# Performance work log

Measured on AMD Instinct MI355X. Metric: run time of the kernel, lower is better.

Reference implementation:

```python
import jax, jax.numpy as jnp
import numpy as np


def setup_inputs() -> dict:
    key = jax.random.key(0)
    k1, k2, k3, k4, k5 = jax.random.split(key, 5)
    N, IN, OUT = 4096, 2048, 2048
    return {
        "input": jax.random.normal(k1, (N, IN), dtype=jnp.float32),
        "weight_mu": jax.random.normal(k2, (OUT, IN), dtype=jnp.float32) * 0.25,
        "weight_rho": jax.random.normal(k3, (OUT, IN), dtype=jnp.float32) - 5.0,
        "eps_weight": jax.random.normal(k4, (OUT, IN), dtype=jnp.float32),
        "bias": jax.random.normal(k5, (OUT,), dtype=jnp.float32) * 0.02,
    }


def reference(input, weight_mu, weight_rho, eps_weight, bias):
    # Effective weight: mu + softplus(rho) * eps   (log1p(exp(rho)) == softplus)
    w = weight_mu + jax.nn.softplus(weight_rho) * eps_weight  # [out, in]
    # F.linear: input @ w.T + bias
    return jnp.einsum("ni,oi->no", input, w) + bias
```

## Files before the change

### kernel.cpp

```cpp
#include <hip/hip_runtime.h>
#include <stdint.h>

typedef __bf16 bf16x8 __attribute__((ext_vector_type(8)));
typedef float f32x4 __attribute__((ext_vector_type(4)));
typedef float float4v __attribute__((ext_vector_type(4)));
typedef unsigned short u16x8 __attribute__((ext_vector_type(8)));

__device__ __forceinline__ unsigned short f2bf(float f) {
    unsigned u = __float_as_uint(f);
    u += 0x7fffu + ((u >> 16) & 1u);
    return (unsigned short)(u >> 16);
}

__device__ __forceinline__ float softplus(float x) {
    return fmaxf(x, 0.0f) + __logf(1.0f + __expf(-fabsf(x)));
}

__device__ __forceinline__ void gl_lds16(const void* gptr, void* lptr) {
    auto g = reinterpret_cast<const __attribute__((address_space(1))) void*>(
        reinterpret_cast<uintptr_t>(gptr));
    auto l = reinterpret_cast<__attribute__((address_space(3))) void*>(
        reinterpret_cast<uintptr_t>(lptr));
    __builtin_amdgcn_global_load_lds(g, l, 16, 0, 0);
}

__global__ void prep_kernel(const float* __restrict__ in,
                            const float* __restrict__ mu,
                            const float* __restrict__ rho,
                            const float* __restrict__ eps,
                            unsigned short* __restrict__ in_bf,
                            unsigned short* __restrict__ w_bf,
                            int nIn8, int nW8) {
    int i = blockIdx.x * blockDim.x + threadIdx.x;
    if (i < nIn8) {
        const float4v* p = (const float4v*)in + (size_t)i * 2;
        float4v a = p[0], b = p[1];
        u16x8 r;
        r[0] = f2bf(a[0]); r[1] = f2bf(a[1]); r[2] = f2bf(a[2]); r[3] = f2bf(a[3]);
        r[4] = f2bf(b[0]); r[5] = f2bf(b[1]); r[6] = f2bf(b[2]); r[7] = f2bf(b[3]);
        ((u16x8*)in_bf)[i] = r;
    } else {
        int j = i - nIn8;
        if (j >= nW8) return;
        const float4v* pm = (const float4v*)mu  + (size_t)j * 2;
        const float4v* pr = (const float4v*)rho + (size_t)j * 2;
        const float4v* pe = (const float4v*)eps + (size_t)j * 2;
        float4v m0 = pm[0], m1 = pm[1];
        float4v r0 = pr[0], r1 = pr[1];
        float4v e0 = pe[0], e1 = pe[1];
        u16x8 r;
        r[0] = f2bf(m0[0] + softplus(r0[0]) * e0[0]);
        r[1] = f2bf(m0[1] + softplus(r0[1]) * e0[1]);
        r[2] = f2bf(m0[2] + softplus(r0[2]) * e0[2]);
        r[3] = f2bf(m0[3] + softplus(r0[3]) * e0[3]);
        r[4] = f2bf(m1[0] + softplus(r1[0]) * e1[0]);
        r[5] = f2bf(m1[1] + softplus(r1[1]) * e1[1]);
        r[6] = f2bf(m1[2] + softplus(r1[2]) * e1[2]);
        r[7] = f2bf(m1[3] + softplus(r1[3]) * e1[3]);
        ((u16x8*)w_bf)[j] = r;
    }
}

#define BM 256
#define BN 128
#define KC 32
#define BUF_U 12288

__global__ __launch_bounds__(512, 4)
void gemm_bt_kernel(const unsigned short* __restrict__ A,
                    const unsigned short* __restrict__ B,
                    const float* __restrict__ bias,
                    float* __restrict__ C,
                    int M, int N, int K) {
    __shared__ unsigned short lds[2][BUF_U];

    const int t      = threadIdx.x;
    const int lane   = t & 63;
    const int wave   = t >> 6;
    const int lane16 = lane & 15;
    const int quad   = lane >> 4;
    const int wm     = wave & 3;
    const int wn     = wave >> 2;

    const int m0 = blockIdx.y * BM;
    const int n0 = blockIdx.x * BN;

    const int r   = t >> 2;
    const int key = (t >> 3) & 3;
    const int kgs = ((t & 3) ^ key) * 8;

    const unsigned short* aP0 = A + (size_t)(m0 + r)       * K + kgs;
    const unsigned short* aP1 = A + (size_t)(m0 + 128 + r) * K + kgs;
    const unsigned short* bP  = B + (size_t)(n0 + r)       * K + kgs;

    f32x4 acc[4][4] = {};

    auto stage = [&](int buf, int it) {
        const int k0 = it * KC;
        gl_lds16(aP0 + k0, &lds[buf][t * 8]);
        gl_lds16(aP1 + k0, &lds[buf][4096 + t * 8]);
        gl_lds16(bP  + k0, &lds[buf][8192 + t * 8]);
    };

    const int sw = (lane16 >> 1) & 3;
    const int ra = (wm * 64 + lane16) * KC + ((quad ^ sw) * 8);
    const int rb = 8192 + (wn * 64 + lane16) * KC + ((quad ^ sw) * 8);

    const int nit = K / KC;
    stage(0, 0);
    __syncthreads();

    auto body = [&](int cur, int it) {
        const unsigned short* la = lds[cur];
        bf16x8 af[4], bfr[4];
#pragma unroll
        for (int mi = 0; mi < 4; ++mi)
            af[mi] = *(const bf16x8*)(la + ra + mi * 16 * KC);
#pragma unroll
        for (int ni = 0; ni < 4; ++ni)
            bfr[ni] = *(const bf16x8*)(la + rb + ni * 16 * KC);
        if (it + 1 < nit) stage(cur ^ 1, it + 1);
        __builtin_amdgcn_s_setprio(1);
#pragma unroll
        for (int mi = 0; mi < 4; ++mi)
#pragma unroll
            for (int ni = 0; ni < 4; ++ni)
                acc[mi][ni] = __builtin_amdgcn_mfma_f32_16x16x32_bf16(
                    af[mi], bfr[ni], acc[mi][ni], 0, 0, 0);
        __builtin_amdgcn_s_setprio(0);
        __syncthreads();
    };

    for (int it = 0; it < nit; it += 2) {
        body(0, it);
        body(1, it + 1);
    }

    float bv[4];
#pragma unroll
    for (int ni = 0; ni < 4; ++ni)
        bv[ni] = bias[n0 + wn * 64 + ni * 16 + lane16];

#pragma unroll
    for (int mi = 0; mi < 4; ++mi) {
        const int rbase = m0 + wm * 64 + mi * 16 + quad * 4;
#pragma unroll
        for (int ni = 0; ni < 4; ++ni) {
            const int col = n0 + wn * 64 + ni * 16 + lane16;
#pragma unroll
            for (int rr = 0; rr < 4; ++rr)
                C[(size_t)(rbase + rr) * N + col] = acc[mi][ni][rr] + bv[ni];
        }
    }
}

extern "C" void kernel_launch(void* const* d_in, const int* in_sizes, int n_in,
                              void* d_out, int out_size, void* d_ws, size_t ws_size,
                              hipStream_t stream) {
    const float* input = (const float*)d_in[0];
    const float* mu    = (const float*)d_in[1];
    const float* rho   = (const float*)d_in[2];
    const float* eps   = (const float*)d_in[3];
    const float* bias  = (const float*)d_in[4];
    float* out = (float*)d_out;

    const int OUT = in_sizes[4];
    const int IN  = in_sizes[1] / OUT;
    const int M   = in_sizes[0] / IN;

    unsigned short* in_bf = (unsigned short*)d_ws;
    unsigned short* w_bf  = in_bf + (size_t)M * IN;

    const int nIn8 = (M * IN) / 8;
    const int nW8  = (OUT * IN) / 8;
    prep_kernel<<<dim3((nIn8 + nW8 + 255) / 256), 256, 0, stream>>>(
        input, mu, rho, eps, in_bf, w_bf, nIn8, nW8);

    gemm_bt_kernel<<<dim3(OUT / BN, M / BM), 512, 0, stream>>>(
        in_bf, w_bf, bias, out, M, OUT, IN);
}
```

Before: 171.2 us.

## Switch GEMM to 128x128 tile with in-block split-K across wave halves

The block tile shrinks from 256x128 to 128x128 and each K step grows from 32 to 64. The two halves of the 8 waves each compute over a different 32-wide K half, and their partial accumulators are combined through LDS in an epilogue. This doubles the grid size to improve occupancy and load balance across CUs, and halves the barriers per K. The cost is lower arithmetic intensity per block, extra LDS traffic and barriers for the reduction, and the removal of the setprio hints.

```diff
diff --git a/kernel.cpp b/kernel.cpp
--- a/kernel.cpp
+++ b/kernel.cpp
@@ -61,10 +61,10 @@
     }
 }
 
-#define BM 256
+#define BM 128
 #define BN 128
-#define KC 32
-#define BUF_U 12288
+#define BK 64
+#define EX_S 66
 
 __global__ __launch_bounds__(512, 4)
 void gemm_bt_kernel(const unsigned short* __restrict__ A,
@@ -72,62 +72,66 @@
                     const float* __restrict__ bias,
                     float* __restrict__ C,
                     int M, int N, int K) {
-    __shared__ unsigned short lds[2][BUF_U];
+    __shared__ unsigned short smem[32768];
+    unsigned short* lds_a0 = smem;
+    unsigned short* lds_b0 = smem + 16384;
 
     const int t      = threadIdx.x;
     const int lane   = t & 63;
     const int wave   = t >> 6;
     const int lane16 = lane & 15;
     const int quad   = lane >> 4;
-    const int wm     = wave & 3;
-    const int wn     = wave >> 2;
+    const int wq     = wave & 3;
+    const int kh     = wave >> 2;
+    const int wm     = wq & 1;
+    const int wn     = wq >> 1;
 
     const int m0 = blockIdx.y * BM;
     const int n0 = blockIdx.x * BN;
 
-    const int r   = t >> 2;
-    const int key = (t >> 3) & 3;
-    const int kgs = ((t & 3) ^ key) * 8;
-
-    const unsigned short* aP0 = A + (size_t)(m0 + r)       * K + kgs;
-    const unsigned short* aP1 = A + (size_t)(m0 + 128 + r) * K + kgs;
-    const unsigned short* bP  = B + (size_t)(n0 + r)       * K + kgs;
+    const int r1   = t >> 3;
+    const int pkg1 = t & 7;
+    const int g1   = (pkg1 ^ (r1 & 7)) * 8;
+    const int r2   = r1 + 64;
+    const int g2   = (pkg1 ^ (r2 & 7)) * 8;
+
+    const unsigned short* Ab = A + (size_t)m0 * K;
+    const unsigned short* Bb = B + (size_t)n0 * K;
 
     f32x4 acc[4][4] = {};
 
-    auto stage = [&](int buf, int it) {
-        const int k0 = it * KC;
-        gl_lds16(aP0 + k0, &lds[buf][t * 8]);
-        gl_lds16(aP1 + k0, &lds[buf][4096 + t * 8]);
-        gl_lds16(bP  + k0, &lds[buf][8192 + t * 8]);
+    auto stage = [&](int buf, int k0) {
+        gl_lds16(Ab + (size_t)r1 * K + k0 + g1, lds_a0 + buf * 8192 + t * 8);
+        gl_lds16(Ab + (size_t)r2 * K + k0 + g2, lds_a0 + buf * 8192 + 4096 + t * 8);
+        gl_lds16(Bb + (size_t)r1 * K + k0 + g1, lds_b0 + buf * 8192 + t * 8);
+        gl_lds16(Bb + (size_t)r2 * K + k0 + g2, lds_b0 + buf * 8192 + 4096 + t * 8);
     };
 
-    const int sw = (lane16 >> 1) & 3;
-    const int ra = (wm * 64 + lane16) * KC + ((quad ^ sw) * 8);
-    const int rb = 8192 + (wn * 64 + lane16) * KC + ((quad ^ sw) * 8);
-
-    const int nit = K / KC;
+    const int sw = lane16 & 7;
+    const int raBase = (wm * 64 + lane16) * BK + (((kh * 4 + quad) ^ sw) * 8);
+    const int rbBase = (wn * 64 + lane16) * BK + (((kh * 4 + quad) ^ sw) * 8);
+
+    const int nit = K / BK;
     stage(0, 0);
     __syncthreads();
 
     auto body = [&](int cur, int it) {
-        const unsigned short* la = lds[cur];
+        const unsigned short* la = lds_a0 + cur * 8192;
+        const unsigned short* lb = lds_b0 + cur * 8192;
         bf16x8 af[4], bfr[4];
 #pragma unroll
         for (int mi = 0; mi < 4; ++mi)
-            af[mi] = *(const bf16x8*)(la + ra + mi * 16 * KC);
+            af[mi] = *(const bf16x8*)(la + raBase + mi * 16 * BK);
 #pragma unroll
         for (int ni = 0; ni < 4; ++ni)
-            bfr[ni] = *(const bf16x8*)(la + rb + ni * 16 * KC);
-        if (it + 1 < nit) stage(cur ^ 1, it + 1);
-        __builtin_amdgcn_s_setprio(1);
+            bfr[ni] = *(const bf16x8*)(lb + rbBase + ni * 16 * BK);
+        if (it + 1 < nit) stage(cur ^ 1, (it + 1) * BK);
 #pragma unroll
         for (int mi = 0; mi < 4; ++mi)
 #pragma unroll
             for (int ni = 0; ni < 4; ++ni)
                 acc[mi][ni] = __builtin_amdgcn_mfma_f32_16x16x32_bf16(
                     af[mi], bfr[ni], acc[mi][ni], 0, 0, 0);
-        __builtin_amdgcn_s_setprio(0);
         __syncthreads();
     };
 
@@ -135,6 +139,37 @@
         body(0, it);
         body(1, it + 1);
     }
+
+    float* fs = (float*)smem;
+#pragma unroll
+    for (int ph = 0; ph < 2; ++ph) {
+        const bool mine = (wq >> 1) == ph;
+        const int rbase0 = (wq & 1) * (64 * EX_S);
+        if (kh == 1 && mine) {
+#pragma unroll
+            for (int mi = 0; mi < 4; ++mi)
+#pragma unroll
+                for (int ni = 0; ni < 4; ++ni)
+#pragma unroll
+                    for (int rr = 0; rr < 4; ++rr)
+                        fs[rbase0 + (mi * 16 + quad * 4 + rr) * EX_S +
+                           ni * 16 + lane16] = acc[mi][ni][rr];
+        }
+        __syncthreads();
+        if (kh == 0 && mine) {
+#pragma unroll
+            for (int mi = 0; mi < 4; ++mi)
+#pragma unroll
+                for (int ni = 0; ni < 4; ++ni)
+#pragma unroll
+                    for (int rr = 0; rr < 4; ++rr)
+                        acc[mi][ni][rr] += fs[rbase0 +
+                            (mi * 16 + quad * 4 + rr) * EX_S + ni * 16 + lane16];
+        }
+        __syncthreads();
+    }
+
+    if (kh != 0) return;
 
     float bv[4];
 #pragma unroll
```

Result: faster. 159.3 us (-6.9%).

## Deepen GEMM LDS pipeline to four slots with vmcnt-based waits

Applied to the files above, without the earlier changes.

Replaces the double-buffered LDS pipeline with a four-slot ring held in dynamic shared memory (96 KB). Loads are issued up to three K-chunks ahead and the kernel waits with explicit vmcnt/lgkmcnt counters and raw s_barrier instead of __syncthreads. The aim is to hide global-load latency better behind the MFMA work. In exchange, launch bounds drop to 2 blocks per CU, so occupancy falls, and the tail iterations reload the last chunk redundantly.

```diff
diff --git a/kernel.cpp b/kernel.cpp
--- a/kernel.cpp
+++ b/kernel.cpp
@@ -63,16 +63,15 @@
 
 #define BM 256
 #define BN 128
-#define KC 32
-#define BUF_U 12288
+#define SLOT_U 12288
 
-__global__ __launch_bounds__(512, 4)
+__global__ __launch_bounds__(512, 2)
 void gemm_bt_kernel(const unsigned short* __restrict__ A,
                     const unsigned short* __restrict__ B,
                     const float* __restrict__ bias,
                     float* __restrict__ C,
                     int M, int N, int K) {
-    __shared__ unsigned short lds[2][BUF_U];
+    extern __shared__ unsigned short smem[];
 
     const int t      = threadIdx.x;
     const int lane   = t & 63;
@@ -85,55 +84,65 @@
     const int m0 = blockIdx.y * BM;
     const int n0 = blockIdx.x * BN;
 
-    const int r   = t >> 2;
+    const int rS  = t >> 2;
     const int key = (t >> 3) & 3;
     const int kgs = ((t & 3) ^ key) * 8;
 
-    const unsigned short* aP0 = A + (size_t)(m0 + r)       * K + kgs;
-    const unsigned short* aP1 = A + (size_t)(m0 + 128 + r) * K + kgs;
-    const unsigned short* bP  = B + (size_t)(n0 + r)       * K + kgs;
+    const unsigned short* aR0 = A + (size_t)(m0 + rS)       * K + kgs;
+    const unsigned short* aR1 = A + (size_t)(m0 + 128 + rS) * K + kgs;
+    const unsigned short* bR  = B + (size_t)(n0 + rS)       * K + kgs;
+
+    auto stage = [&](int slot, int k0) {
+        unsigned short* s = smem + slot * SLOT_U;
+        gl_lds16(aR0 + k0, s + t * 8);
+        gl_lds16(aR1 + k0, s + 4096 + t * 8);
+        gl_lds16(bR  + k0, s + 8192 + t * 8);
+    };
+
+    const int sw  = (lane16 >> 1) & 3;
+    const int pk  = (quad ^ sw) * 8;
+    const int oA0 = (wm * 64 + lane16) * 32 + pk;
+    const int oB0 = 8192 + (wn * 64 + lane16) * 32 + pk;
 
     f32x4 acc[4][4] = {};
 
-    auto stage = [&](int buf, int it) {
-        const int k0 = it * KC;
-        gl_lds16(aP0 + k0, &lds[buf][t * 8]);
-        gl_lds16(aP1 + k0, &lds[buf][4096 + t * 8]);
-        gl_lds16(bP  + k0, &lds[buf][8192 + t * 8]);
-    };
-
-    const int sw = (lane16 >> 1) & 3;
-    const int ra = (wm * 64 + lane16) * KC + ((quad ^ sw) * 8);
-    const int rb = 8192 + (wn * 64 + lane16) * KC + ((quad ^ sw) * 8);
-
-    const int nit = K / KC;
-    stage(0, 0);
-    __syncthreads();
-
-    auto body = [&](int cur, int it) {
-        const unsigned short* la = lds[cur];
-        bf16x8 af[4], bfr[4];
+    auto phase = [&](const unsigned short* sl, int stageSlot, int stageK0) {
+        bf16x8 af[4], bf[4];
 #pragma unroll
         for (int mi = 0; mi < 4; ++mi)
-            af[mi] = *(const bf16x8*)(la + ra + mi * 16 * KC);
+            af[mi] = *(const bf16x8*)(sl + oA0 + mi * 512);
 #pragma unroll
         for (int ni = 0; ni < 4; ++ni)
-            bfr[ni] = *(const bf16x8*)(la + rb + ni * 16 * KC);
-        if (it + 1 < nit) stage(cur ^ 1, it + 1);
+            bf[ni] = *(const bf16x8*)(sl + oB0 + ni * 512);
+        stage(stageSlot, stageK0);
+        asm volatile("s_waitcnt lgkmcnt(0)" ::: "memory");
+        __builtin_amdgcn_sched_barrier(0);
         __builtin_amdgcn_s_setprio(1);
 #pragma unroll
         for (int mi = 0; mi < 4; ++mi)
 #pragma unroll
             for (int ni = 0; ni < 4; ++ni)
                 acc[mi][ni] = __builtin_amdgcn_mfma_f32_16x16x32_bf16(
-                    af[mi], bfr[ni], acc[mi][ni], 0, 0, 0);
+                    af[mi], bf[ni], acc[mi][ni], 0, 0, 0);
         __builtin_amdgcn_s_setprio(0);
-        __syncthreads();
+        __builtin_amdgcn_s_barrier();
     };
 
-    for (int it = 0; it < nit; it += 2) {
-        body(0, it);
-        body(1, it + 1);
+    const int nt = K / 64;
+    stage(0, 0);
+    stage(1, 32);
+    stage(2, 64);
+
+    for (int tt = 0; tt < nt; ++tt) {
+        const int d = tt & 1;
+        asm volatile("s_waitcnt vmcnt(3)" ::: "memory");
+        __builtin_amdgcn_sched_barrier(0);
+        __builtin_amdgcn_s_barrier();
+        __builtin_amdgcn_sched_barrier(0);
+        const int sA = ((tt + 1 < nt) ? (tt + 1) : (nt - 1)) * 64 + 32;
+        phase(smem + (d * 2) * SLOT_U, (d ^ 1) * 2 + 1, sA);
+        const int sB = ((tt + 2 < nt) ? (tt + 2) : (nt - 1)) * 64;
+        phase(smem + (d * 2 + 1) * SLOT_U, d * 2, sB);
     }
 
     float bv[4];
@@ -171,11 +180,19 @@
     unsigned short* in_bf = (unsigned short*)d_ws;
     unsigned short* w_bf  = in_bf + (size_t)M * IN;
 
+    static bool attr_done = false;
+    if (!attr_done) {
+        (void)hipFuncSetAttribute(
+            reinterpret_cast<const void*>(&gemm_bt_kernel),
+            hipFuncAttributeMaxDynamicSharedMemorySize, 4 * SLOT_U * 2);
+        attr_done = true;
+    }
+
     const int nIn8 = (M * IN) / 8;
     const int nW8  = (OUT * IN) / 8;
     prep_kernel<<<dim3((nIn8 + nW8 + 255) / 256), 256, 0, stream>>>(
         input, mu, rho, eps, in_bf, w_bf, nIn8, nW8);
 
-    gemm_bt_kernel<<<dim3(OUT / BN, M / BM), 512, 0, stream>>>(
+    gemm_bt_kernel<<<dim3(OUT / BN, M / BM), 512, 4 * SLOT_U * 2, stream>>>(
         in_bf, w_bf, bias, out, M, OUT, IN);
 }
```

Result: faster. 161.7 us (-5.5%).
